# Performance work log

Measured on AMD Instinct MI355X. Metric: run time of the kernel, lower is better.

Reference implementation:

```python
import jax, jax.numpy as jnp
import numpy as np

B, N_SMI, N_ATOM, N_PROT, D = 8, 100, 45, 1000, 64


def setup_inputs() -> dict:
    key = jax.random.key(0)
    ks = jax.random.split(key, 8)
    return {
        "smi_tf": jax.random.normal(ks[0], (B, N_SMI, D), dtype=jnp.float32),
        "pro_tf": jax.random.normal(ks[1], (B, N_PROT, D), dtype=jnp.float32),
        "drug_gat": jax.random.normal(ks[2], (B, N_ATOM, D), dtype=jnp.float32),
        "w_att": jax.random.normal(ks[3], (D, D), dtype=jnp.float32) * 0.05,
        "b_att": jnp.zeros((D,), dtype=jnp.float32),
        "w1": jax.random.normal(ks[4], (2 * D, 1024), dtype=jnp.float32) * 0.05,
        "b1": jnp.zeros((1024,), dtype=jnp.float32),
        "w2": jax.random.normal(ks[5], (1024, 1024), dtype=jnp.float32) * 0.05,
        "b2": jnp.zeros((1024,), dtype=jnp.float32),
        "w3": jax.random.normal(ks[6], (1024, 512), dtype=jnp.float32) * 0.05,
        "b3": jnp.zeros((512,), dtype=jnp.float32),
        "w4": jax.random.normal(ks[7], (512, 2), dtype=jnp.float32) * 0.05,
        "b4": jnp.zeros((2,), dtype=jnp.float32),
    }


def reference(smi_tf, pro_tf, drug_gat, w_att, b_att, w1, b1, w2, b2, w3, b3, w4, b4):
    # shared attention projection on both streams
    smi_att = smi_tf @ w_att + b_att            # (B, N_smi, D)
    pro_att = pro_tf @ w_att + b_att            # (B, N_prot, D)
    smi_attss = jnp.concatenate([smi_att, drug_gat], axis=1)  # (B, Nd, D)

    # pairwise broadcast add + relu + shared linear (the big intermediate)
    pair = jax.nn.relu(smi_attss[:, :, None, :] + pro_att[:, None, :, :])  # (B, Nd, Np, D)
    atten = pair @ w_att + b_att                                           # (B, Nd, Np, D)

    # dual mean-pool gates
    smi_atts = jax.nn.sigmoid(atten.mean(axis=2))   # (B, Nd, D)
    pro_atts = jax.nn.sigmoid(atten.mean(axis=1))   # (B, Np, D)

    smi_tfs = 0.5 * smi_attss + smi_attss * smi_atts
    pro_tfs = 0.5 * pro_tf + pro_tf * pro_atts

    smi = smi_tfs.mean(axis=1)   # (B, D)
    pro = pro_tfs.mean(axis=1)   # (B, D)
    x = jnp.concatenate([smi, pro], axis=-1)  # (B, 2D)

    x = jax.nn.relu(x @ w1 + b1)
    x = jax.nn.relu(x @ w2 + b2)
    x = jax.nn.relu(x @ w3 + b3)
    return x @ w4 + b4  # (B, 2)
```

## Files before the change

kernel.cpp:

```cpp
#include <hip/hip_runtime.h>
#include <math.h>

#define B 8
#define NSMI 100
#define NATOM 45
#define ND 145
#define NP 1000
#define D 64
#define NROW 1145

#define PROJ_RPB 16
#define PROJ_BPB 72
#define ROW_BPB 37
#define COL_BPB 250
#define PAIR_ROW_BLKS (B * ROW_BPB)
#define PAIR_BLKS (PAIR_ROW_BLKS + B * COL_BPB)
#define TAIL_BLKS 128

__device__ __forceinline__ float4 f4z() { float4 z; z.x = z.y = z.z = z.w = 0.f; return z; }
__device__ __forceinline__ void f4acc(float4& a, const float4& v) {
    a.x += v.x; a.y += v.y; a.z += v.z; a.w += v.w;
}
__device__ __forceinline__ void acc_relu(float4& acc, const float4& a, const float4& p) {
    acc.x += fmaxf(0.f, a.x + p.x);
    acc.y += fmaxf(0.f, a.y + p.y);
    acc.z += fmaxf(0.f, a.z + p.z);
    acc.w += fmaxf(0.f, a.w + p.w);
}
__device__ __forceinline__ void wave_red_g(float4& v) {
    v.x += __shfl_xor(v.x, 16, 64); v.x += __shfl_xor(v.x, 32, 64);
    v.y += __shfl_xor(v.y, 16, 64); v.y += __shfl_xor(v.y, 32, 64);
    v.z += __shfl_xor(v.z, 16, 64); v.z += __shfl_xor(v.z, 32, 64);
    v.w += __shfl_xor(v.w, 16, 64); v.w += __shfl_xor(v.w, 32, 64);
}

__device__ __forceinline__ void gridbar(int* bar, int ph, int nblk) {
    __syncthreads();
    if (threadIdx.x == 0) {
        __threadfence();
        __hip_atomic_fetch_add(&bar[ph], 1, __ATOMIC_ACQ_REL, __HIP_MEMORY_SCOPE_AGENT);
        while (__hip_atomic_load(&bar[ph], __ATOMIC_ACQUIRE, __HIP_MEMORY_SCOPE_AGENT) < nblk)
            __builtin_amdgcn_s_sleep(1);
        __threadfence();
    }
    __syncthreads();
}

__global__ __launch_bounds__(256) void k_proj2(
    const float* __restrict__ smi_tf, const float* __restrict__ pro_tf,
    const float* __restrict__ drug_gat, const float* __restrict__ w_att,
    const float* __restrict__ b_att,
    float* __restrict__ smi_attss, float* __restrict__ pro_att, int* __restrict__ bar)
{
    int blk = blockIdx.x, t = threadIdx.x;
    if (blk == 0 && t < 16) bar[t] = 0;
    int b = blk / PROJ_BPB;
    int r0 = (blk - b * PROJ_BPB) * PROJ_RPB;

    __shared__ float4 wl[64 * 17];
    __shared__ float4 rl4[16 * 17];

    #pragma unroll
    for (int i2 = 0; i2 < 4; ++i2) {
        int f = t + 256 * i2;
        float4 v = ((const float4*)w_att)[f];
        wl[(f >> 4) * 17 + (f & 15)] = v;
    }
    int rl = t >> 4, p = t & 15;
    int r = r0 + rl;
    {
        float4 v = f4z();
        if (r < NROW) {
            const float* src;
            if (r < NSMI)      src = smi_tf   + (size_t)(b * NSMI + r) * D;
            else if (r < ND)   src = drug_gat + (size_t)(b * NATOM + (r - NSMI)) * D;
            else               src = pro_tf   + (size_t)(b * NP + (r - ND)) * D;
            v = ((const float4*)src)[p];
        }
        rl4[rl * 17 + p] = v;
    }
    __syncthreads();
    if (r >= NROW) return;
    float4 out;
    if (r >= NSMI && r < ND) {
        out = rl4[rl * 17 + p];
    } else {
        float4 acc = ((const float4*)b_att)[p];
        const float* rowf = (const float*)rl4;
        #pragma unroll
        for (int k = 0; k < 64; ++k) {
            float val = rowf[rl * 68 + k];
            float4 w = wl[k * 17 + p];
            acc.x = fmaf(val, w.x, acc.x);
            acc.y = fmaf(val, w.y, acc.y);
            acc.z = fmaf(val, w.z, acc.z);
            acc.w = fmaf(val, w.w, acc.w);
        }
        out = acc;
    }
    if (r < ND) ((float4*)smi_attss)[(size_t)(b * ND + r) * 16 + p] = out;
    else        ((float4*)pro_att)[(size_t)(b * NP + (r - ND)) * 16 + p] = out;
}

__global__ __launch_bounds__(512) void k_pair(
    const float4* __restrict__ smi4, const float4* __restrict__ pro4,
    const float* __restrict__ smi_attss, const float* __restrict__ pro_tf,
    const float* __restrict__ w_att, const float* __restrict__ b_att,
    float* __restrict__ smi_tfs, float* __restrict__ pro_tfs)
{
    __shared__ float4 red[8][4][16];
    __shared__ float vl[4][64];
    int blk = blockIdx.x, t = threadIdx.x;
    int w = t >> 6, lane = t & 63, l = lane & 15, g = lane >> 4;
    int u = w * 4 + g;
    float4 acc0 = f4z(), acc1 = f4z(), acc2 = f4z(), acc3 = f4z();
    int b, base;
    bool isRow = (blk < PAIR_ROW_BLKS);

    if (isRow) {
        b = blk / ROW_BPB;
        base = (blk - b * ROW_BPB) * 4;
        float4 a0 = (base + 0 < ND) ? smi4[(size_t)(b * ND + base + 0) * 16 + l] : f4z();
        float4 a1 = (base + 1 < ND) ? smi4[(size_t)(b * ND + base + 1) * 16 + l] : f4z();
        float4 a2 = (base + 2 < ND) ? smi4[(size_t)(b * ND + base + 2) * 16 + l] : f4z();
        float4 a3 = (base + 3 < ND) ? smi4[(size_t)(b * ND + base + 3) * 16 + l] : f4z();
        const float4* pp = pro4 + (size_t)b * NP * 16 + u * 16 + l;
        #pragma unroll 4
        for (int it = 0; it < 31; ++it) {
            float4 pv = pp[it * 512];
            acc_relu(acc0, a0, pv); acc_relu(acc1, a1, pv);
            acc_relu(acc2, a2, pv); acc_relu(acc3, a3, pv);
        }
        if (u < 8) {
            float4 pv = pp[31 * 512];
            acc_relu(acc0, a0, pv); acc_relu(acc1, a1, pv);
            acc_relu(acc2, a2, pv); acc_relu(acc3, a3, pv);
        }
    } else {
        int cb = blk - PAIR_ROW_BLKS;
        b = cb / COL_BPB;
        base = (cb - b * COL_BPB) * 4;
        float4 p0 = pro4[(size_t)(b * NP + base + 0) * 16 + l];
        float4 p1 = pro4[(size_t)(b * NP + base + 1) * 16 + l];
        float4 p2 = pro4[(size_t)(b * NP + base + 2) * 16 + l];
        float4 p3 = pro4[(size_t)(b * NP + base + 3) * 16 + l];
        const float4* ap = smi4 + (size_t)b * ND * 16 + u * 16 + l;
        #pragma unroll
        for (int it = 0; it < 4; ++it) {
            float4 av = ap[it * 512];
            acc_relu(acc0, av, p0); acc_relu(acc1, av, p1);
            acc_relu(acc2, av, p2); acc_relu(acc3, av, p3);
        }
        if (u < 17) {
            float4 av = ap[4 * 512];
            acc_relu(acc0, av, p0); acc_relu(acc1, av, p1);
            acc_relu(acc2, av, p2); acc_relu(acc3, av, p3);
        }
    }

    wave_red_g(acc0); wave_red_g(acc1); wave_red_g(acc2); wave_red_g(acc3);
    if (lane < 16) {
        red[w][0][l] = acc0; red[w][1][l] = acc1;
        red[w][2][l] = acc2; red[w][3][l] = acc3;
    }
    __syncthreads();
    float invn = isRow ? (1.0f / NP) : (1.0f / ND);
    if (t < 64) {
        int ii = t >> 4, l2 = t & 15;
        float4 s = f4z();
        #pragma unroll
        for (int w2 = 0; w2 < 8; ++w2) f4acc(s, red[w2][ii][l2]);
        vl[ii][l2 * 4 + 0] = s.x * invn;
        vl[ii][l2 * 4 + 1] = s.y * invn;
        vl[ii][l2 * 4 + 2] = s.z * invn;
        vl[ii][l2 * 4 + 3] = s.w * invn;
    }
    __syncthreads();
    if (t < 256) {
        int ii = t >> 6, d = t & 63;
        int r = base + ii;
        bool ok = isRow ? (r < ND) : true;
        if (ok) {
            float m = b_att[d];
            #pragma unroll
            for (int k = 0; k < 64; ++k) m = fmaf(vl[ii][k], w_att[k * 64 + d], m);
            float gs = 1.f / (1.f + expf(-m));
            if (isRow) {
                size_t idx = (size_t)(b * ND + r) * 64 + d;
                smi_tfs[idx] = smi_attss[idx] * (0.5f + gs);
            } else {
                size_t idx = (size_t)(b * NP + r) * 64 + d;
                pro_tfs[idx] = pro_tf[idx] * (0.5f + gs);
            }
        }
    }
}

__global__ __launch_bounds__(512) void k_tail(
    const float4* __restrict__ smi_tfs4, const float4* __restrict__ pro_tfs4,
    const float* __restrict__ w1, const float* __restrict__ b1,
    const float* __restrict__ w2, const float* __restrict__ b2,
    const float* __restrict__ w3, const float* __restrict__ b3,
    const float* __restrict__ w4p, const float* __restrict__ b4p,
    float* __restrict__ x, float* __restrict__ h1, float* __restrict__ h2,
    float* __restrict__ h3, int* __restrict__ bar, float* __restrict__ out)
{
    __shared__ float4 ldsb[1024];
    float* lds = (float*)ldsb;
    int blk = blockIdx.x, t = threadIdx.x;

    {
        int b = blk >> 4, s = blk & 15;
        float4 sa = f4z(), pa = f4z();
        if (t < ND) f4acc(sa, smi_tfs4[(size_t)(b * ND + t) * 16 + s]);
        for (int j = t; j < NP; j += 512) f4acc(pa, pro_tfs4[(size_t)(b * NP + j) * 16 + s]);
        ldsb[t] = sa; ldsb[512 + t] = pa;
        __syncthreads();
        for (int st = 256; st > 0; st >>= 1) {
            if (t < st) { f4acc(ldsb[t], ldsb[t + st]); f4acc(ldsb[512 + t], ldsb[512 + t + st]); }
            __syncthreads();
        }
        if (t == 0) {
            float4 S = ldsb[0], P = ldsb[512];
            x[b * 128 + s * 4 + 0] = S.x * (1.0f / ND);
            x[b * 128 + s * 4 + 1] = S.y * (1.0f / ND);
            x[b * 128 + s * 4 + 2] = S.z * (1.0f / ND);
            x[b * 128 + s * 4 + 3] = S.w * (1.0f / ND);
            x[b * 128 + 64 + s * 4 + 0] = P.x * (1.0f / NP);
            x[b * 128 + 64 + s * 4 + 1] = P.y * (1.0f / NP);
            x[b * 128 + 64 + s * 4 + 2] = P.z * (1.0f / NP);
            x[b * 128 + 64 + s * 4 + 3] = P.w * (1.0f / NP);
        }
    }
    gridbar(bar, 0, TAIL_BLKS);

    {
        int b = blk >> 4, och = blk & 15;
        int ol = t & 63, kc = t >> 6;
        int o = och * 64 + ol;
        const float* xr = x + b * 128 + kc * 16;
        const float* wp = w1 + (size_t)(kc * 16) * 1024 + o;
        float acc = 0.f;
        #pragma unroll
        for (int k = 0; k < 16; ++k) acc = fmaf(xr[k], wp[(size_t)k * 1024], acc);
        lds[t] = acc;
        __syncthreads();
        if (t < 64) {
            float v = b1[och * 64 + t];
            #pragma unroll
            for (int c = 0; c < 8; ++c) v += lds[c * 64 + t];
            h1[b * 1024 + och * 64 + t] = fmaxf(v, 0.f);
        }
    }
    gridbar(bar, 1, TAIL_BLKS);

    {
        int b = blk >> 4, och = blk & 15;
        int ol = t & 63, kc = t >> 6;
        int o = och * 64 + ol;
        const float* hp = h1 + b * 1024 + kc * 128;
        const float* wp = w2 + (size_t)(kc * 128) * 1024 + o;
        float acc = 0.f;
        #pragma unroll 8
        for (int k = 0; k < 128; ++k) acc = fmaf(hp[k], wp[(size_t)k * 1024], acc);
        __syncthreads();
        lds[t] = acc;
        __syncthreads();
        if (t < 64) {
            float v = b2[och * 64 + t];
            #pragma unroll
            for (int c = 0; c < 8; ++c) v += lds[c * 64 + t];
            h2[b * 1024 + och * 64 + t] = fmaxf(v, 0.f);
        }
    }
    gridbar(bar, 2, TAIL_BLKS);

    {
        int b = blk >> 4, och = blk & 15;
        int ol = t & 31, kc = t >> 5;
        int o = och * 32 + ol;
        const float* hp = h2 + b * 1024 + kc * 64;
        const float* wp = w3 + (size_t)(kc * 64) * 512 + o;
        float acc = 0.f;
        #pragma unroll 8
        for (int k = 0; k < 64; ++k) acc = fmaf(hp[k], wp[(size_t)k * 512], acc);
        __syncthreads();
        lds[t] = acc;
        __syncthreads();
        if (t < 32) {
            float v = b3[och * 32 + t];
            #pragma unroll
            for (int c = 0; c < 16; ++c) v += lds[c * 32 + t];
            h3[b * 512 + och * 32 + t] = fmaxf(v, 0.f);
        }
    }
    gridbar(bar, 3, TAIL_BLKS);

    if (blk < 8) {
        int b = blk;
        int o = t >> 8, kl = t & 255;
        float acc = h3[b * 512 + kl * 2] * w4p[(kl * 2) * 2 + o]
                  + h3[b * 512 + kl * 2 + 1] * w4p[(kl * 2 + 1) * 2 + o];
        lds[t] = acc;
        __syncthreads();
        for (int st = 128; st > 0; st >>= 1) {
            if (kl < st) lds[o * 256 + kl] += lds[o * 256 + kl + st];
            __syncthreads();
        }
        if (t == 0) {
            out[b * 2 + 0] = lds[0] + b4p[0];
            out[b * 2 + 1] = lds[256] + b4p[1];
        }
    }
}

extern "C" void kernel_launch(void* const* d_in, const int* in_sizes, int n_in,
                              void* d_out, int out_size, void* d_ws, size_t ws_size,
                              hipStream_t stream)
{
    const float* smi_tf   = (const float*)d_in[0];
    const float* pro_tf   = (const float*)d_in[1];
    const float* drug_gat = (const float*)d_in[2];
    const float* w_att    = (const float*)d_in[3];
    const float* b_att    = (const float*)d_in[4];
    const float* w1 = (const float*)d_in[5];
    const float* b1 = (const float*)d_in[6];
    const float* w2 = (const float*)d_in[7];
    const float* b2 = (const float*)d_in[8];
    const float* w3 = (const float*)d_in[9];
    const float* b3 = (const float*)d_in[10];
    const float* w4 = (const float*)d_in[11];
    const float* b4 = (const float*)d_in[12];
    float* out = (float*)d_out;

    float* ws = (float*)d_ws;
    float* smi_attss = ws;
    float* pro_att   = smi_attss + 74240;
    float* smi_tfs   = pro_att + 512000;
    float* pro_tfs   = smi_tfs + 74240;
    float* x   = pro_tfs + 512000;
    float* h1  = x + 1024;
    float* h2  = h1 + 8192;
    float* h3  = h2 + 8192;
    int*   bar = (int*)(h3 + 4096);

    k_proj2<<<B * PROJ_BPB, 256, 0, stream>>>(smi_tf, pro_tf, drug_gat, w_att, b_att,
                                              smi_attss, pro_att, bar);
    k_pair <<<PAIR_BLKS, 512, 0, stream>>>((const float4*)smi_attss, (const float4*)pro_att,
                                           smi_attss, pro_tf, w_att, b_att, smi_tfs, pro_tfs);
    k_tail <<<TAIL_BLKS, 512, 0, stream>>>((const float4*)smi_tfs, (const float4*)pro_tfs,
                                           w1, b1, w2, b2, w3, b3, w4, b4,
                                           x, h1, h2, h3, bar, out);
}
```

Measured before the change: 157.1 us.

## Split MLP tail along K with batch-shared float4 weight loads and deferred reductions

The MLP layers in the tail kernel now split the reduction dimension across blocks. Each block loads every weight row once as float4 and applies it to all 8 batch rows, instead of reloading weights per batch element. Partial sums go to global buffers and are reduced at the start of the next stage, where bias and ReLU are also applied. This cuts redundant weight traffic, especially for the 4 MB w2 matrix, at the cost of larger partial-sum writes and reads. Fewer blocks are active in each stage.

```diff
diff --git a/kernel.cpp b/kernel.cpp
--- a/kernel.cpp
+++ b/kernel.cpp
@@ -198,12 +198,12 @@
 
 __global__ __launch_bounds__(512) void k_tail(
     const float4* __restrict__ smi_tfs4, const float4* __restrict__ pro_tfs4,
-    const float* __restrict__ w1, const float* __restrict__ b1,
-    const float* __restrict__ w2, const float* __restrict__ b2,
-    const float* __restrict__ w3, const float* __restrict__ b3,
+    const float4* __restrict__ w1_4, const float* __restrict__ b1,
+    const float4* __restrict__ w2_4, const float* __restrict__ b2,
+    const float4* __restrict__ w3_4, const float* __restrict__ b3,
     const float* __restrict__ w4p, const float* __restrict__ b4p,
-    float* __restrict__ x, float* __restrict__ h1, float* __restrict__ h2,
-    float* __restrict__ h3, int* __restrict__ bar, float* __restrict__ out)
+    float* __restrict__ x, float* __restrict__ part1, float* __restrict__ part2,
+    float* __restrict__ part3, int* __restrict__ bar, float* __restrict__ out)
 {
     __shared__ float4 ldsb[1024];
     float* lds = (float*)ldsb;
@@ -234,82 +234,133 @@
     }
     gridbar(bar, 0, TAIL_BLKS);
 
-    {
-        int b = blk >> 4, och = blk & 15;
-        int ol = t & 63, kc = t >> 6;
-        int o = och * 64 + ol;
-        const float* xr = x + b * 128 + kc * 16;
-        const float* wp = w1 + (size_t)(kc * 16) * 1024 + o;
-        float acc = 0.f;
-        #pragma unroll
-        for (int k = 0; k < 16; ++k) acc = fmaf(xr[k], wp[(size_t)k * 1024], acc);
-        lds[t] = acc;
-        __syncthreads();
-        if (t < 64) {
-            float v = b1[och * 64 + t];
-            #pragma unroll
-            for (int c = 0; c < 8; ++c) v += lds[c * 64 + t];
-            h1[b * 1024 + och * 64 + t] = fmaxf(v, 0.f);
+    if (blk < 32) {
+        int vc = blk;
+        if (t < 32) {
+            int b = t >> 2, kk = t & 3;
+            lds[t] = x[b * 128 + vc * 4 + kk];
+        }
+        __syncthreads();
+        if (t < 256) {
+            int o4 = t;
+            float4 acc[8];
+            #pragma unroll
+            for (int b = 0; b < 8; ++b) acc[b] = f4z();
+            #pragma unroll
+            for (int kk = 0; kk < 4; ++kk) {
+                float4 wv = w1_4[(size_t)(vc * 4 + kk) * 256 + o4];
+                #pragma unroll
+                for (int b = 0; b < 8; ++b) {
+                    float xv = lds[b * 4 + kk];
+                    acc[b].x = fmaf(xv, wv.x, acc[b].x);
+                    acc[b].y = fmaf(xv, wv.y, acc[b].y);
+                    acc[b].z = fmaf(xv, wv.z, acc[b].z);
+                    acc[b].w = fmaf(xv, wv.w, acc[b].w);
+                }
+            }
+            #pragma unroll
+            for (int b = 0; b < 8; ++b)
+                ((float4*)part1)[(size_t)(vc * 8 + b) * 256 + o4] = acc[b];
         }
     }
     gridbar(bar, 1, TAIL_BLKS);
 
-    {
-        int b = blk >> 4, och = blk & 15;
-        int ol = t & 63, kc = t >> 6;
-        int o = och * 64 + ol;
-        const float* hp = h1 + b * 1024 + kc * 128;
-        const float* wp = w2 + (size_t)(kc * 128) * 1024 + o;
-        float acc = 0.f;
-        #pragma unroll 8
-        for (int k = 0; k < 128; ++k) acc = fmaf(hp[k], wp[(size_t)k * 1024], acc);
-        __syncthreads();
-        lds[t] = acc;
-        __syncthreads();
-        if (t < 64) {
-            float v = b2[och * 64 + t];
-            #pragma unroll
-            for (int c = 0; c < 8; ++c) v += lds[c * 64 + t];
-            h2[b * 1024 + och * 64 + t] = fmaxf(v, 0.f);
+    if (blk < 64) {
+        int vc = blk, kbase = vc * 16;
+        if (t < 256) {
+            int pair = t & 127, half = t >> 7;
+            int b = pair >> 4, kk = pair & 15;
+            const float* pp = part1 + (size_t)(half * 16 * 8 + b) * 1024 + kbase + kk;
+            float s = 0.f;
+            #pragma unroll
+            for (int p = 0; p < 16; ++p) s += pp[(size_t)p * 8192];
+            lds[t] = s;
+        }
+        __syncthreads();
+        if (t < 128) {
+            int b = t >> 4, kk = t & 15;
+            float s = lds[t] + lds[t + 128];
+            lds[256 + t] = fmaxf(0.f, b1[kbase + kk] + s);
+        }
+        __syncthreads();
+        if (t < 256) {
+            int o4 = t;
+            float4 acc[8];
+            #pragma unroll
+            for (int b = 0; b < 8; ++b) acc[b] = f4z();
+            #pragma unroll
+            for (int kk = 0; kk < 16; ++kk) {
+                float4 wv = w2_4[(size_t)(kbase + kk) * 256 + o4];
+                #pragma unroll
+                for (int b = 0; b < 8; ++b) {
+                    float hv = lds[256 + b * 16 + kk];
+                    acc[b].x = fmaf(hv, wv.x, acc[b].x);
+                    acc[b].y = fmaf(hv, wv.y, acc[b].y);
+                    acc[b].z = fmaf(hv, wv.z, acc[b].z);
+                    acc[b].w = fmaf(hv, wv.w, acc[b].w);
+                }
+            }
+            #pragma unroll
+            for (int b = 0; b < 8; ++b)
+                ((float4*)part2)[(size_t)(vc * 8 + b) * 256 + o4] = acc[b];
         }
     }
     gridbar(bar, 2, TAIL_BLKS);
 
-    {
-        int b = blk >> 4, och = blk & 15;
-        int ol = t & 31, kc = t >> 5;
-        int o = och * 32 + ol;
-        const float* hp = h2 + b * 1024 + kc * 64;
-        const float* wp = w3 + (size_t)(kc * 64) * 512 + o;
-        float acc = 0.f;
-        #pragma unroll 8
-        for (int k = 0; k < 64; ++k) acc = fmaf(hp[k], wp[(size_t)k * 512], acc);
-        __syncthreads();
-        lds[t] = acc;
-        __syncthreads();
-        if (t < 32) {
-            float v = b3[och * 32 + t];
-            #pragma unroll
-            for (int c = 0; c < 16; ++c) v += lds[c * 32 + t];
-            h3[b * 512 + och * 32 + t] = fmaxf(v, 0.f);
+    if (blk < 32) {
+        int vc = blk, kbase = vc * 32;
+        if (t < 256) {
+            int b = t >> 5, kk = t & 31;
+            const float* pp = part2 + (size_t)b * 1024 + kbase + kk;
+            float s = 0.f;
+            #pragma unroll 8
+            for (int p = 0; p < 64; ++p) s += pp[(size_t)p * 8192];
+            lds[t] = fmaxf(0.f, b2[kbase + kk] + s);
+        }
+        __syncthreads();
+        if (t < 256) {
+            int o4 = t & 127, ksub = t >> 7;
+            float4 acc[8];
+            #pragma unroll
+            for (int b = 0; b < 8; ++b) acc[b] = f4z();
+            #pragma unroll
+            for (int kk = 0; kk < 16; ++kk) {
+                int k = kbase + ksub * 16 + kk;
+                float4 wv = w3_4[(size_t)k * 128 + o4];
+                #pragma unroll
+                for (int b = 0; b < 8; ++b) {
+                    float hv = lds[b * 32 + ksub * 16 + kk];
+                    acc[b].x = fmaf(hv, wv.x, acc[b].x);
+                    acc[b].y = fmaf(hv, wv.y, acc[b].y);
+                    acc[b].z = fmaf(hv, wv.z, acc[b].z);
+                    acc[b].w = fmaf(hv, wv.w, acc[b].w);
+                }
+            }
+            #pragma unroll
+            for (int b = 0; b < 8; ++b)
+                ((float4*)part3)[(size_t)((vc * 2 + ksub) * 8 + b) * 128 + o4] = acc[b];
         }
     }
     gridbar(bar, 3, TAIL_BLKS);
 
     if (blk < 8) {
         int b = blk;
-        int o = t >> 8, kl = t & 255;
-        float acc = h3[b * 512 + kl * 2] * w4p[(kl * 2) * 2 + o]
-                  + h3[b * 512 + kl * 2 + 1] * w4p[(kl * 2 + 1) * 2 + o];
-        lds[t] = acc;
-        __syncthreads();
-        for (int st = 128; st > 0; st >>= 1) {
-            if (kl < st) lds[o * 256 + kl] += lds[o * 256 + kl + st];
+        int o = t;
+        const float* pp = part3 + (size_t)b * 512 + o;
+        float s = 0.f;
+        #pragma unroll 8
+        for (int p = 0; p < 64; ++p) s += pp[(size_t)p * 4096];
+        float h = fmaxf(0.f, b3[o] + s);
+        lds[t] = h * w4p[o * 2 + 0];
+        lds[512 + t] = h * w4p[o * 2 + 1];
+        __syncthreads();
+        for (int st = 256; st > 0; st >>= 1) {
+            if (t < st) { lds[t] += lds[t + st]; lds[512 + t] += lds[512 + t + st]; }
             __syncthreads();
         }
         if (t == 0) {
             out[b * 2 + 0] = lds[0] + b4p[0];
-            out[b * 2 + 1] = lds[256] + b4p[1];
+            out[b * 2 + 1] = lds[512] + b4p[1];
         }
     }
 }
@@ -338,17 +389,18 @@
     float* pro_att   = smi_attss + 74240;
     float* smi_tfs   = pro_att + 512000;
     float* pro_tfs   = smi_tfs + 74240;
-    float* x   = pro_tfs + 512000;
-    float* h1  = x + 1024;
-    float* h2  = h1 + 8192;
-    float* h3  = h2 + 8192;
-    int*   bar = (int*)(h3 + 4096);
+    float* x     = pro_tfs + 512000;
+    float* part1 = x + 1024;
+    float* part2 = part1 + 262144;
+    float* part3 = part2 + 524288;
+    int*   bar  = (int*)(part3 + 262144);
 
     k_proj2<<<B * PROJ_BPB, 256, 0, stream>>>(smi_tf, pro_tf, drug_gat, w_att, b_att,
                                               smi_attss, pro_att, bar);
     k_pair <<<PAIR_BLKS, 512, 0, stream>>>((const float4*)smi_attss, (const float4*)pro_att,
                                            smi_attss, pro_tf, w_att, b_att, smi_tfs, pro_tfs);
     k_tail <<<TAIL_BLKS, 512, 0, stream>>>((const float4*)smi_tfs, (const float4*)pro_tfs,
-                                           w1, b1, w2, b2, w3, b3, w4, b4,
-                                           x, h1, h2, h3, bar, out);
-}
+                                           (const float4*)w1, b1, (const float4*)w2, b2,
+                                           (const float4*)w3, b3, w4, b4,
+                                           x, part1, part2, part3, bar, out);
+}
```

After: 181.9 us. 15.8% more time.
